# Kernel tuning notes

Measured on AMD Instinct MI355X. Metric: run time of the kernel, lower is better.

## Reference

```python
import jax, jax.numpy as jnp
import numpy as np

UNITS = 256  # LSTM hidden size per source (units=256)

def setup_inputs() -> dict:
    key = jax.random.key(0)
    ks = jax.random.split(key, 7)
    vocab, embed_dim, seq_len, batch, n_cls = 50000, 256, 512, 64, 20
    x = jax.random.randint(ks[0], (batch, seq_len), 0, vocab)
    emb = jax.random.normal(ks[1], (vocab, embed_dim), jnp.float32) * 0.05
    W = jax.random.normal(ks[2], (embed_dim, 4 * UNITS), jnp.float32) * (1.0 / np.sqrt(embed_dim))
    U = jax.random.normal(ks[3], (UNITS, 4 * UNITS), jnp.float32) * (1.0 / np.sqrt(UNITS))
    # keras unit_forget_bias: forget-gate bias = 1, others 0 (gate order i,f,c,o)
    b = jnp.concatenate([jnp.zeros((UNITS,)), jnp.ones((UNITS,)), jnp.zeros((2 * UNITS,))]).astype(jnp.float32)
    Wd = jax.random.normal(ks[4], (UNITS, n_cls), jnp.float32) * (1.0 / np.sqrt(UNITS))
    bd = jnp.zeros((n_cls,), jnp.float32)
    return {"x": x, "emb": emb, "W": W, "U": U, "b": b, "Wd": Wd, "bd": bd}

def reference(x, emb, W, U, b, Wd, bd):
    # Embedding lookup: [B, T] -> [B, T, D]
    e = emb[x]
    B = e.shape[0]
    # Pre-compute input projections for all timesteps (one big GEMM): [B, T, 4H]
    xz = jnp.einsum('btd,dh->bth', e, W) + b
    h0 = jnp.zeros((B, UNITS), e.dtype)
    c0 = jnp.zeros((B, UNITS), e.dtype)

    def step(carry, zt):
        h, c = carry
        z = zt + h @ U  # [B, 4H]
        i, f, g, o = jnp.split(z, 4, axis=-1)
        i = jax.nn.sigmoid(i)
        f = jax.nn.sigmoid(f)
        g = jnp.tanh(g)
        o = jax.nn.sigmoid(o)
        c_new = f * c + i * g
        h_new = o * jnp.tanh(c_new)
        return (h_new, c_new), None

    (h_T, _), _ = jax.lax.scan(step, (h0, c0), jnp.swapaxes(xz, 0, 1))
    logits = h_T @ Wd + bd
    return jax.nn.softmax(logits, axis=-1)
```

## Files before the change

### kernel.cpp

```cpp
#include <hip/hip_runtime.h>
#include <hip/hip_bf16.h>
#include <math.h>


typedef __bf16 bf16_t;
typedef bf16_t bf16x8 __attribute__((ext_vector_type(8)));
typedef bf16_t bf16x4 __attribute__((ext_vector_type(4)));
typedef float  f32x4  __attribute__((ext_vector_type(4)));
typedef unsigned long long u64;

#define T_SZ 512
#define HID 256
#define G4 1024
#define NCLS 20

#define WS_UPACK 0u
#define WS_WPACK (512u * 1024u)
#define WS_HFIN  (1024u * 1024u)
#define WS_EXCH  (1536u * 1024u)
#define WS_XZ    (2u * 1024u * 1024u)

__global__ void pack_weights(const float* __restrict__ W, const float* __restrict__ U,
                             bf16_t* __restrict__ Wp, bf16_t* __restrict__ Up) {
    int tid  = blockIdx.x * blockDim.x + threadIdx.x;
    int j    = tid & 7;
    int lane = (tid >> 3) & 63;
    int ks   = (tid >> 9) & 7;
    int nt   = tid >> 12;
    int row  = ks * 32 + ((lane >> 4) << 3) + j;
    int col  = nt * 16 + (lane & 15);
    Wp[tid] = (bf16_t)W[row * G4 + col];
    Up[tid] = (bf16_t)U[row * G4 + col];
}

__global__ __launch_bounds__(256) void xz_gemm(const int* __restrict__ x,
                                               const float* __restrict__ emb,
                                               const bf16_t* __restrict__ Wp,
                                               const float* __restrict__ bias,
                                               bf16x4* __restrict__ xz2) {
    int nb   = blockIdx.x & 7;
    int t    = blockIdx.x >> 3;
    int w    = threadIdx.x >> 6;
    int lane = threadIdx.x & 63;
    int l15  = lane & 15;
    int quad = lane >> 4;

    int b_row = w * 16 + l15;
    int tok   = x[b_row * T_SZ + t];
    const float* erow = emb + (size_t)tok * 256;

    bf16x8 afrag[8];
#pragma unroll
    for (int ks = 0; ks < 8; ks++) {
        const float4* p = (const float4*)(erow + ks * 32 + quad * 8);
        float4 v0 = p[0], v1 = p[1];
        bf16x8 a;
        a[0] = (bf16_t)v0.x; a[1] = (bf16_t)v0.y; a[2] = (bf16_t)v0.z; a[3] = (bf16_t)v0.w;
        a[4] = (bf16_t)v1.x; a[5] = (bf16_t)v1.y; a[6] = (bf16_t)v1.z; a[7] = (bf16_t)v1.w;
        afrag[ks] = a;
    }

    const bf16x8* Wf = (const bf16x8*)Wp;

#pragma unroll
    for (int nt = 0; nt < 8; nt++) {
        int ntg = nb * 8 + nt;
        float bv = bias[ntg * 16 + l15];
        f32x4 acc = {bv, bv, bv, bv};
        const bf16x8* bp = Wf + (size_t)(ntg * 8) * 64 + lane;
#pragma unroll
        for (int ks = 0; ks < 8; ks++) {
            bf16x8 bfrag = bp[ks * 64];
            acc = __builtin_amdgcn_mfma_f32_16x16x32_bf16(afrag[ks], bfrag, acc, 0, 0, 0);
        }
        bf16x4 hv;
#pragma unroll
        for (int r = 0; r < 4; r++) hv[r] = (bf16_t)acc[r];
        xz2[((size_t)(t * 4 + w) * 64 + ntg) * 64 + lane] = hv;
    }
}

__device__ __forceinline__ float sigmoid_f(float z) {
    return 1.0f / (1.0f + __expf(-z));
}
__device__ __forceinline__ float tanh_f(float z) {
    float e = __expf(2.0f * z);
    return 1.0f - 2.0f / (e + 1.0f);
}
__device__ __forceinline__ unsigned pack2(float a, float b) {
    unsigned short xs = __builtin_bit_cast(unsigned short, (bf16_t)a);
    unsigned short ys = __builtin_bit_cast(unsigned short, (bf16_t)b);
    return (unsigned)xs | ((unsigned)ys << 16);
}
__device__ __forceinline__ bf16_t unpk_lo(unsigned v) {
    return __builtin_bit_cast(bf16_t, (unsigned short)(v & 0xffffu));
}
__device__ __forceinline__ bf16_t unpk_hi(unsigned v) {
    return __builtin_bit_cast(bf16_t, (unsigned short)(v >> 16));
}

__device__ __forceinline__ void mfma_aB(f32x4& d, bf16x8 a, bf16x8 b) {
    asm("v_mfma_f32_16x16x32_bf16 %0, %1, %2, %0" : "+v"(d) : "v"(a), "a"(b));
}

__global__ __launch_bounds__(512, 2) void lstm_pair(const bf16x4* __restrict__ xz2,
                                                    const bf16_t* __restrict__ Up,
                                                    u64* __restrict__ exch,
                                                    float* __restrict__ hfin) {
    if (blockIdx.x & 4) return;
    const int g    = blockIdx.x & 3;
    const int p    = (blockIdx.x >> 3) & 1;
    const int w    = threadIdx.x >> 6;
    const int lane = threadIdx.x & 63;
    const int l15  = lane & 15;
    const int quad = lane >> 4;

    __shared__ __align__(16) bf16_t h_lds[2][16][264];

    const bf16x8* Uf = (const bf16x8*)Up + lane;
    bf16x8 u[4][8];
#pragma unroll
    for (int G = 0; G < 4; G++) {
        int ntg = G * 16 + p * 8 + w;
#pragma unroll
        for (int ks = 0; ks < 8; ks++)
            u[G][ks] = Uf[(ntg * 8 + ks) * 64];
    }
    asm volatile("" : "+a"(u[0][0]), "+a"(u[0][1]), "+a"(u[0][2]), "+a"(u[0][3]),
                      "+a"(u[0][4]), "+a"(u[0][5]), "+a"(u[0][6]), "+a"(u[0][7]));
    asm volatile("" : "+a"(u[1][0]), "+a"(u[1][1]), "+a"(u[1][2]), "+a"(u[1][3]),
                      "+a"(u[1][4]), "+a"(u[1][5]), "+a"(u[1][6]), "+a"(u[1][7]));
    asm volatile("" : "+a"(u[2][0]), "+a"(u[2][1]), "+a"(u[2][2]), "+a"(u[2][3]),
                      "+a"(u[2][4]), "+a"(u[2][5]), "+a"(u[2][6]), "+a"(u[2][7]));
    asm volatile("" : "+a"(u[3][0]), "+a"(u[3][1]), "+a"(u[3][2]), "+a"(u[3][3]),
                      "+a"(u[3][4]), "+a"(u[3][5]), "+a"(u[3][6]), "+a"(u[3][7]));

    for (int i = threadIdx.x; i < 2 * 16 * 264; i += 512)
        (&h_lds[0][0][0])[i] = (bf16_t)0.0f;

    f32x4 cst = {0.f, 0.f, 0.f, 0.f};

    bf16x4 xzv[4];
#pragma unroll
    for (int G = 0; G < 4; G++)
        xzv[G] = xz2[((size_t)(0 * 4 + g) * 64 + (G * 16 + p * 8 + w)) * 64 + lane];

    __syncthreads();

    for (int t = 0; t < T_SZ; t++) {
        const int buf  = t & 1;
        const int nbuf = buf ^ 1;
        const unsigned key = ((unsigned)(t >> 3) + 1u) << 24;

        bf16x8 af[8];
#pragma unroll
        for (int ks = 0; ks < 8; ks++)
            af[ks] = *(const bf16x8*)&h_lds[buf][l15][ks * 32 + quad * 8];

        f32x4 acc[4];
#pragma unroll
        for (int G = 0; G < 4; G++) {
            bf16x4 xv = xzv[G];
            f32x4 a = {(float)xv[0], (float)xv[1], (float)xv[2], (float)xv[3]};
            acc[G] = a;
        }
#pragma unroll
        for (int ks = 0; ks < 8; ks++)
#pragma unroll
            for (int G = 0; G < 4; G++)
                mfma_aB(acc[G], af[ks], u[G][ks]);

        if (t + 1 < T_SZ) {
#pragma unroll
            for (int G = 0; G < 4; G++)
                xzv[G] = xz2[((size_t)((t + 1) * 4 + g) * 64 + (G * 16 + p * 8 + w)) * 64 + lane];
        }

        float hv[4];
#pragma unroll
        for (int r = 0; r < 4; r++) {
            float ig = sigmoid_f(acc[0][r]);
            float fg = sigmoid_f(acc[1][r]);
            float gg = tanh_f(acc[2][r]);
            float og = sigmoid_f(acc[3][r]);
            float cn = fg * cst[r] + ig * gg;
            cst[r] = cn;
            hv[r] = og * tanh_f(cn);
        }

        if (t == T_SZ - 1) {
#pragma unroll
            for (int r = 0; r < 4; r++)
                hfin[(g * 16 + quad * 4 + r) * HID + p * 128 + w * 16 + l15] = hv[r];
            break;
        }

        {
            unsigned dw0 = pack2(hv[0], hv[1]);
            unsigned dw1 = pack2(hv[2], hv[3]);
            u64 q0 = (u64)dw0 | ((u64)(dw0 ^ key) << 32);
            u64 q1 = (u64)dw1 | ((u64)(dw1 ^ key) << 32);
            unsigned base = (((unsigned)(t & 7) * 4 + (unsigned)g) * 2 + (unsigned)p) * 1024u;
            unsigned ui   = (unsigned)(w * 16 + l15) * 8u + (unsigned)(quad * 2);
            __hip_atomic_store(&exch[base + ui],     q0, __ATOMIC_RELAXED, __HIP_MEMORY_SCOPE_AGENT);
            __hip_atomic_store(&exch[base + ui + 1], q1, __ATOMIC_RELAXED, __HIP_MEMORY_SCOPE_AGENT);
        }

#pragma unroll
        for (int r = 0; r < 4; r++)
            h_lds[nbuf][quad * 4 + r][p * 128 + w * 16 + l15] = (bf16_t)hv[r];

        asm volatile("s_waitcnt vmcnt(0)" ::: "memory");

        {
            unsigned pbase = (((unsigned)(t & 7) * 4 + (unsigned)g) * 2 + (unsigned)(1 - p)) * 1024u;
            unsigned i0 = (unsigned)threadIdx.x * 2u;
            u64 q0, q1;
            for (;;) {
                q0 = __hip_atomic_load(&exch[pbase + i0],     __ATOMIC_RELAXED, __HIP_MEMORY_SCOPE_AGENT);
                q1 = __hip_atomic_load(&exch[pbase + i0 + 1], __ATOMIC_RELAXED, __HIP_MEMORY_SCOPE_AGENT);
                bool v0 = ((unsigned)(q0 >> 32)) == (((unsigned)q0) ^ key);
                bool v1 = ((unsigned)(q1 >> 32)) == (((unsigned)q1) ^ key);
                if (v0 && v1) break;
            }
            unsigned d0 = (unsigned)q0, d1 = (unsigned)q1;
            int ul  = (int)(i0 >> 3);
            int qq  = (int)((i0 & 7) >> 1);
            int col = (1 - p) * 128 + ul;
            h_lds[nbuf][qq * 4 + 0][col] = unpk_lo(d0);
            h_lds[nbuf][qq * 4 + 1][col] = unpk_hi(d0);
            h_lds[nbuf][qq * 4 + 2][col] = unpk_lo(d1);
            h_lds[nbuf][qq * 4 + 3][col] = unpk_hi(d1);
        }

        __syncthreads();
    }
}

__global__ void head(const float* __restrict__ hfin, const float* __restrict__ Wd,
                     const float* __restrict__ bd, float* __restrict__ out) {
    __shared__ float hrow[HID];
    __shared__ float lg[32];
    __shared__ float ex[32];
    int b = blockIdx.x, tid = threadIdx.x;
    for (int i = tid; i < HID; i += 64) hrow[i] = hfin[b * HID + i];
    __syncthreads();
    if (tid < NCLS) {
        float acc = bd[tid];
        for (int k = 0; k < HID; k++) acc = fmaf(hrow[k], Wd[k * NCLS + tid], acc);
        lg[tid] = acc;
    }
    __syncthreads();
    if (tid < NCLS) {
        float m = -1e30f;
        for (int jj = 0; jj < NCLS; jj++) m = fmaxf(m, lg[jj]);
        ex[tid] = __expf(lg[tid] - m);
    }
    __syncthreads();
    if (tid < NCLS) {
        float sden = 0.0f;
        for (int jj = 0; jj < NCLS; jj++) sden += ex[jj];
        out[b * NCLS + tid] = ex[tid] / sden;
    }
}

extern "C" void kernel_launch(void* const* d_in, const int* in_sizes, int n_in,
                              void* d_out, int out_size, void* d_ws, size_t ws_size,
                              hipStream_t stream) {
    const int*   x    = (const int*)d_in[0];
    const float* emb  = (const float*)d_in[1];
    const float* W    = (const float*)d_in[2];
    const float* U    = (const float*)d_in[3];
    const float* bias = (const float*)d_in[4];
    const float* Wd   = (const float*)d_in[5];
    const float* bd   = (const float*)d_in[6];
    float* out = (float*)d_out;

    char* ws = (char*)d_ws;
    bf16_t* Up   = (bf16_t*)(ws + WS_UPACK);
    bf16_t* Wp   = (bf16_t*)(ws + WS_WPACK);
    float*  hf   = (float*)(ws + WS_HFIN);
    u64*    exch = (u64*)(ws + WS_EXCH);
    bf16x4* xz2  = (bf16x4*)(ws + WS_XZ);

    pack_weights<<<dim3(1024), dim3(256), 0, stream>>>(W, U, Wp, Up);
    xz_gemm<<<dim3(4096), dim3(256), 0, stream>>>(x, emb, Wp, bias, xz2);
    lstm_pair<<<dim3(16), dim3(512), 0, stream>>>(xz2, Up, exch, hf);
    head<<<dim3(64), dim3(64), 0, stream>>>(hf, Wd, bd, out);
}
```

Baseline: 1.412 ms.

## Process two batch groups per workgroup to overlap exchange latency

Each active workgroup now handles two 16-row batch groups (A and B) instead of one, halving the number of active blocks from 8 to 4. Group A's hidden state is published to the partner block before group B's MFMA and gate math run, so the cross-block exchange latency can hide behind B's compute. The xz prefetch moves after the store wait, and the spin loops gain an iteration guard. In exchange, each block does twice the serial work per step, and the guard can silently proceed with stale data if it expires.

```diff
diff --git a/kernel.cpp b/kernel.cpp
--- a/kernel.cpp
+++ b/kernel.cpp
@@ -107,15 +107,17 @@
                                                     const bf16_t* __restrict__ Up,
                                                     u64* __restrict__ exch,
                                                     float* __restrict__ hfin) {
-    if (blockIdx.x & 4) return;
-    const int g    = blockIdx.x & 3;
+    if (blockIdx.x & 6) return;
+    const int gg   = blockIdx.x & 1;
+    const int gA   = gg * 2;
+    const int gB   = gA + 1;
     const int p    = (blockIdx.x >> 3) & 1;
     const int w    = threadIdx.x >> 6;
     const int lane = threadIdx.x & 63;
     const int l15  = lane & 15;
     const int quad = lane >> 4;
 
-    __shared__ __align__(16) bf16_t h_lds[2][16][264];
+    __shared__ __align__(16) bf16_t h_lds[2][2][16][264];
 
     const bf16x8* Uf = (const bf16x8*)Up + lane;
     bf16x8 u[4][8];
@@ -135,17 +137,26 @@
     asm volatile("" : "+a"(u[3][0]), "+a"(u[3][1]), "+a"(u[3][2]), "+a"(u[3][3]),
                       "+a"(u[3][4]), "+a"(u[3][5]), "+a"(u[3][6]), "+a"(u[3][7]));
 
-    for (int i = threadIdx.x; i < 2 * 16 * 264; i += 512)
-        (&h_lds[0][0][0])[i] = (bf16_t)0.0f;
-
-    f32x4 cst = {0.f, 0.f, 0.f, 0.f};
-
-    bf16x4 xzv[4];
-#pragma unroll
-    for (int G = 0; G < 4; G++)
-        xzv[G] = xz2[((size_t)(0 * 4 + g) * 64 + (G * 16 + p * 8 + w)) * 64 + lane];
+    for (int i = threadIdx.x; i < 2 * 2 * 16 * 264; i += 512)
+        (&h_lds[0][0][0][0])[i] = (bf16_t)0.0f;
+
+    f32x4 cstA = {0.f, 0.f, 0.f, 0.f};
+    f32x4 cstB = {0.f, 0.f, 0.f, 0.f};
+
+    bf16x4 xzvA[4], xzvB[4];
+#pragma unroll
+    for (int G = 0; G < 4; G++) {
+        xzvA[G] = xz2[((size_t)(0 * 4 + gA) * 64 + (G * 16 + p * 8 + w)) * 64 + lane];
+        xzvB[G] = xz2[((size_t)(0 * 4 + gB) * 64 + (G * 16 + p * 8 + w)) * 64 + lane];
+    }
 
     __syncthreads();
+
+    const unsigned i0 = (unsigned)threadIdx.x * 2u;
+    const unsigned ui = (unsigned)(w * 16 + l15) * 8u + (unsigned)(quad * 2);
+    const int ul  = (int)(i0 >> 3);
+    const int qq  = (int)((i0 & 7) >> 1);
+    const int pcol = (1 - p) * 128 + ul;
 
     for (int t = 0; t < T_SZ; t++) {
         const int buf  = t & 1;
@@ -155,82 +166,141 @@
         bf16x8 af[8];
 #pragma unroll
         for (int ks = 0; ks < 8; ks++)
-            af[ks] = *(const bf16x8*)&h_lds[buf][l15][ks * 32 + quad * 8];
-
-        f32x4 acc[4];
+            af[ks] = *(const bf16x8*)&h_lds[0][buf][l15][ks * 32 + quad * 8];
+
+        f32x4 accA[4];
 #pragma unroll
         for (int G = 0; G < 4; G++) {
-            bf16x4 xv = xzv[G];
+            bf16x4 xv = xzvA[G];
             f32x4 a = {(float)xv[0], (float)xv[1], (float)xv[2], (float)xv[3]};
-            acc[G] = a;
+            accA[G] = a;
         }
 #pragma unroll
         for (int ks = 0; ks < 8; ks++)
 #pragma unroll
             for (int G = 0; G < 4; G++)
-                mfma_aB(acc[G], af[ks], u[G][ks]);
+                mfma_aB(accA[G], af[ks], u[G][ks]);
+
+        float hvA[4];
+#pragma unroll
+        for (int r = 0; r < 4; r++) {
+            float ig = sigmoid_f(accA[0][r]);
+            float fg = sigmoid_f(accA[1][r]);
+            float gv = tanh_f(accA[2][r]);
+            float og = sigmoid_f(accA[3][r]);
+            float cn = fg * cstA[r] + ig * gv;
+            cstA[r] = cn;
+            hvA[r] = og * tanh_f(cn);
+        }
 
         if (t + 1 < T_SZ) {
-#pragma unroll
-            for (int G = 0; G < 4; G++)
-                xzv[G] = xz2[((size_t)((t + 1) * 4 + g) * 64 + (G * 16 + p * 8 + w)) * 64 + lane];
-        }
-
-        float hv[4];
-#pragma unroll
-        for (int r = 0; r < 4; r++) {
-            float ig = sigmoid_f(acc[0][r]);
-            float fg = sigmoid_f(acc[1][r]);
-            float gg = tanh_f(acc[2][r]);
-            float og = sigmoid_f(acc[3][r]);
-            float cn = fg * cst[r] + ig * gg;
-            cst[r] = cn;
-            hv[r] = og * tanh_f(cn);
-        }
-
-        if (t == T_SZ - 1) {
-#pragma unroll
-            for (int r = 0; r < 4; r++)
-                hfin[(g * 16 + quad * 4 + r) * HID + p * 128 + w * 16 + l15] = hv[r];
-            break;
-        }
-
-        {
-            unsigned dw0 = pack2(hv[0], hv[1]);
-            unsigned dw1 = pack2(hv[2], hv[3]);
+            unsigned dw0 = pack2(hvA[0], hvA[1]);
+            unsigned dw1 = pack2(hvA[2], hvA[3]);
             u64 q0 = (u64)dw0 | ((u64)(dw0 ^ key) << 32);
             u64 q1 = (u64)dw1 | ((u64)(dw1 ^ key) << 32);
-            unsigned base = (((unsigned)(t & 7) * 4 + (unsigned)g) * 2 + (unsigned)p) * 1024u;
-            unsigned ui   = (unsigned)(w * 16 + l15) * 8u + (unsigned)(quad * 2);
+            unsigned base = (((unsigned)(t & 7) * 4 + (unsigned)gA) * 2 + (unsigned)p) * 1024u;
             __hip_atomic_store(&exch[base + ui],     q0, __ATOMIC_RELAXED, __HIP_MEMORY_SCOPE_AGENT);
             __hip_atomic_store(&exch[base + ui + 1], q1, __ATOMIC_RELAXED, __HIP_MEMORY_SCOPE_AGENT);
-        }
-
-#pragma unroll
-        for (int r = 0; r < 4; r++)
-            h_lds[nbuf][quad * 4 + r][p * 128 + w * 16 + l15] = (bf16_t)hv[r];
+#pragma unroll
+            for (int r = 0; r < 4; r++)
+                h_lds[0][nbuf][quad * 4 + r][p * 128 + w * 16 + l15] = (bf16_t)hvA[r];
+            __builtin_amdgcn_sched_barrier(0);
+        }
+
+#pragma unroll
+        for (int ks = 0; ks < 8; ks++)
+            af[ks] = *(const bf16x8*)&h_lds[1][buf][l15][ks * 32 + quad * 8];
+
+        f32x4 accB[4];
+#pragma unroll
+        for (int G = 0; G < 4; G++) {
+            bf16x4 xv = xzvB[G];
+            f32x4 a = {(float)xv[0], (float)xv[1], (float)xv[2], (float)xv[3]};
+            accB[G] = a;
+        }
+#pragma unroll
+        for (int ks = 0; ks < 8; ks++)
+#pragma unroll
+            for (int G = 0; G < 4; G++)
+                mfma_aB(accB[G], af[ks], u[G][ks]);
+
+        float hvB[4];
+#pragma unroll
+        for (int r = 0; r < 4; r++) {
+            float ig = sigmoid_f(accB[0][r]);
+            float fg = sigmoid_f(accB[1][r]);
+            float gv = tanh_f(accB[2][r]);
+            float og = sigmoid_f(accB[3][r]);
+            float cn = fg * cstB[r] + ig * gv;
+            cstB[r] = cn;
+            hvB[r] = og * tanh_f(cn);
+        }
+
+        if (t == T_SZ - 1) {
+#pragma unroll
+            for (int r = 0; r < 4; r++) {
+                hfin[(gA * 16 + quad * 4 + r) * HID + p * 128 + w * 16 + l15] = hvA[r];
+                hfin[(gB * 16 + quad * 4 + r) * HID + p * 128 + w * 16 + l15] = hvB[r];
+            }
+            break;
+        }
+
+        {
+            unsigned dw0 = pack2(hvB[0], hvB[1]);
+            unsigned dw1 = pack2(hvB[2], hvB[3]);
+            u64 q0 = (u64)dw0 | ((u64)(dw0 ^ key) << 32);
+            u64 q1 = (u64)dw1 | ((u64)(dw1 ^ key) << 32);
+            unsigned base = (((unsigned)(t & 7) * 4 + (unsigned)gB) * 2 + (unsigned)p) * 1024u;
+            __hip_atomic_store(&exch[base + ui],     q0, __ATOMIC_RELAXED, __HIP_MEMORY_SCOPE_AGENT);
+            __hip_atomic_store(&exch[base + ui + 1], q1, __ATOMIC_RELAXED, __HIP_MEMORY_SCOPE_AGENT);
+#pragma unroll
+            for (int r = 0; r < 4; r++)
+                h_lds[1][nbuf][quad * 4 + r][p * 128 + w * 16 + l15] = (bf16_t)hvB[r];
+        }
+        __builtin_amdgcn_sched_barrier(0);
 
         asm volatile("s_waitcnt vmcnt(0)" ::: "memory");
+#pragma unroll
+        for (int G = 0; G < 4; G++) {
+            xzvA[G] = xz2[((size_t)((t + 1) * 4 + gA) * 64 + (G * 16 + p * 8 + w)) * 64 + lane];
+            xzvB[G] = xz2[((size_t)((t + 1) * 4 + gB) * 64 + (G * 16 + p * 8 + w)) * 64 + lane];
+        }
 
         {
-            unsigned pbase = (((unsigned)(t & 7) * 4 + (unsigned)g) * 2 + (unsigned)(1 - p)) * 1024u;
-            unsigned i0 = (unsigned)threadIdx.x * 2u;
+            unsigned pbase = (((unsigned)(t & 7) * 4 + (unsigned)gA) * 2 + (unsigned)(1 - p)) * 1024u;
             u64 q0, q1;
+            unsigned guard = 0;
             for (;;) {
                 q0 = __hip_atomic_load(&exch[pbase + i0],     __ATOMIC_RELAXED, __HIP_MEMORY_SCOPE_AGENT);
                 q1 = __hip_atomic_load(&exch[pbase + i0 + 1], __ATOMIC_RELAXED, __HIP_MEMORY_SCOPE_AGENT);
                 bool v0 = ((unsigned)(q0 >> 32)) == (((unsigned)q0) ^ key);
                 bool v1 = ((unsigned)(q1 >> 32)) == (((unsigned)q1) ^ key);
                 if (v0 && v1) break;
+                if (++guard > (1u << 22)) break;
             }
             unsigned d0 = (unsigned)q0, d1 = (unsigned)q1;
-            int ul  = (int)(i0 >> 3);
-            int qq  = (int)((i0 & 7) >> 1);
-            int col = (1 - p) * 128 + ul;
-            h_lds[nbuf][qq * 4 + 0][col] = unpk_lo(d0);
-            h_lds[nbuf][qq * 4 + 1][col] = unpk_hi(d0);
-            h_lds[nbuf][qq * 4 + 2][col] = unpk_lo(d1);
-            h_lds[nbuf][qq * 4 + 3][col] = unpk_hi(d1);
+            h_lds[0][nbuf][qq * 4 + 0][pcol] = unpk_lo(d0);
+            h_lds[0][nbuf][qq * 4 + 1][pcol] = unpk_hi(d0);
+            h_lds[0][nbuf][qq * 4 + 2][pcol] = unpk_lo(d1);
+            h_lds[0][nbuf][qq * 4 + 3][pcol] = unpk_hi(d1);
+        }
+        {
+            unsigned pbase = (((unsigned)(t & 7) * 4 + (unsigned)gB) * 2 + (unsigned)(1 - p)) * 1024u;
+            u64 q0, q1;
+            unsigned guard = 0;
+            for (;;) {
+                q0 = __hip_atomic_load(&exch[pbase + i0],     __ATOMIC_RELAXED, __HIP_MEMORY_SCOPE_AGENT);
+                q1 = __hip_atomic_load(&exch[pbase + i0 + 1], __ATOMIC_RELAXED, __HIP_MEMORY_SCOPE_AGENT);
+                bool v0 = ((unsigned)(q0 >> 32)) == (((unsigned)q0) ^ key);
+                bool v1 = ((unsigned)(q1 >> 32)) == (((unsigned)q1) ^ key);
+                if (v0 && v1) break;
+                if (++guard > (1u << 22)) break;
+            }
+            unsigned d0 = (unsigned)q0, d1 = (unsigned)q1;
+            h_lds[1][nbuf][qq * 4 + 0][pcol] = unpk_lo(d0);
+            h_lds[1][nbuf][qq * 4 + 1][pcol] = unpk_hi(d0);
+            h_lds[1][nbuf][qq * 4 + 2][pcol] = unpk_lo(d1);
+            h_lds[1][nbuf][qq * 4 + 3][pcol] = unpk_hi(d1);
         }
 
         __syncthreads();
```

Result: slower. 2.672 ms (+89.3%).
